# Optimization experiments

Measured on AMD Instinct MI355X. Metric: run time of the kernel, lower is better.

Reference implementation:

```python
import jax, jax.numpy as jnp
import numpy as np

N_HEADS = 16
D_EMBD = 1024
D_HEAD = D_EMBD // N_HEADS  # 64


def setup_inputs() -> dict:
    key = jax.random.key(0)
    k0, k1, k2, k3, k4 = jax.random.split(key, 5)
    s = 1.0 / np.sqrt(D_EMBD)
    return {
        "x": jax.random.normal(k0, (4, 2048, D_EMBD), dtype=jnp.float32),
        "w_in": jax.random.normal(k1, (D_EMBD, 3 * D_EMBD), dtype=jnp.float32) * s,
        "b_in": jax.random.normal(k2, (3 * D_EMBD,), dtype=jnp.float32) * 0.02,
        "w_out": jax.random.normal(k3, (D_EMBD, D_EMBD), dtype=jnp.float32) * s,
        "b_out": jax.random.normal(k4, (D_EMBD,), dtype=jnp.float32) * 0.02,
    }


def reference(x, w_in, b_in, w_out, b_out):
    B, S, D = x.shape
    # fused QKV projection; torch .chunk(3) order in source is k, q, v
    kqv = x @ w_in + b_in                      # [B, S, 3D]
    k, q, v = jnp.split(kqv, 3, axis=-1)
    # split heads: [B, S, D] -> [B, H, S, Dh]
    def heads(t):
        return t.reshape(B, S, N_HEADS, D_HEAD).transpose(0, 2, 1, 3)
    q, k, v = heads(q), heads(k), heads(v)
    # attention scores, explicit O(S^2) matrix (naive, unmasked path)
    scores = jnp.einsum("bhsd,bhtd->bhst", q, k) / jnp.sqrt(
        jnp.asarray(D_HEAD, dtype=x.dtype)
    )
    probs = jax.nn.softmax(scores, axis=-1)    # [B, H, S, S]
    out = jnp.einsum("bhst,bhtd->bhsd", probs, v)
    out = out.transpose(0, 2, 1, 3).reshape(B, S, D)
    return out @ w_out + b_out
```

## Files before the change

### kernel.cpp

```cpp
#include <hip/hip_runtime.h>

typedef unsigned short u16;
typedef __attribute__((ext_vector_type(8))) short bf16x8;
typedef __attribute__((ext_vector_type(4))) float f32x4;

#define MFMA(a, b, c) __builtin_amdgcn_mfma_f32_16x16x32_bf16(a, b, c, 0, 0, 0)

#if defined(__has_builtin)
#if __has_builtin(__builtin_amdgcn_exp2f)
#define EXP2(x) __builtin_amdgcn_exp2f(x)
#endif
#endif
#ifndef EXP2
#define EXP2(x) exp2f(x)
#endif

#define ASYNC16(g, l)                                                      \
  __builtin_amdgcn_global_load_lds(                                        \
      (const __attribute__((address_space(1))) void*)(g),                  \
      (__attribute__((address_space(3))) void*)(l), 16, 0, 0)

#define SEQ 2048
#define KQW 2048

__device__ __forceinline__ u16 f2bf(float x) {
  union { float f; unsigned u; } v; v.f = x;
  unsigned r = (v.u + 0x7fffu + ((v.u >> 16) & 1u)) >> 16;
  return (u16)r;
}

__device__ __forceinline__ unsigned pack_bf2(float a, float b) {
  unsigned ua = __float_as_uint(a) + 0x8000u;
  unsigned ub = __float_as_uint(b) + 0x8000u;
  return __builtin_amdgcn_perm(ub, ua, 0x07060302u);
}

__device__ __forceinline__ bf16x8 exp_pack8(const f32x4 a, const f32x4 b) {
  union { unsigned u[4]; bf16x8 v; } r;
  r.u[0] = pack_bf2(EXP2(a[0]), EXP2(a[1]));
  r.u[1] = pack_bf2(EXP2(a[2]), EXP2(a[3]));
  r.u[2] = pack_bf2(EXP2(b[0]), EXP2(b[1]));
  r.u[3] = pack_bf2(EXP2(b[2]), EXP2(b[3]));
  return r.v;
}

__global__ __launch_bounds__(256) void prep_fused(const float* __restrict__ w_in,
                                                  u16* __restrict__ wT_in,
                                                  const float* __restrict__ w_out,
                                                  u16* __restrict__ wT_out,
                                                  const float4* __restrict__ x,
                                                  uint2* __restrict__ xb) {
  int bid = blockIdx.x;
  int tid = threadIdx.x;
  if (bid >= 4096) {
    int idx = (bid - 4096) * 256 + tid;
    float4 v = x[idx];
    xb[idx] = make_uint2(pack_bf2(v.x, v.y), pack_bf2(v.z, v.w));
    return;
  }
  const float* in;
  u16* out;
  int R = 1024, C, bx, by;
  if (bid < 3072) {
    in = w_in; out = wT_in; C = 3072; bx = bid % 96; by = bid / 96;
  } else {
    int b2 = bid - 3072;
    in = w_out; out = wT_out; C = 1024; bx = b2 & 31; by = b2 >> 5;
  }
  __shared__ float tile[32][33];
  int tx = tid & 31, ty = tid >> 5;
  int c0 = bx * 32, r0 = by * 32;
#pragma unroll
  for (int i = 0; i < 32; i += 8)
    tile[ty + i][tx] = in[(size_t)(r0 + ty + i) * C + c0 + tx];
  __syncthreads();
#pragma unroll
  for (int i = 0; i < 32; i += 8)
    out[(size_t)(c0 + ty + i) * R + r0 + tx] = f2bf(tile[tx][ty + i]);
}

#define BM 128
#define BN 128
#define BK 64

template <int MODE, int NBX>
__global__ __launch_bounds__(256, 2) void gemm_bt(const u16* __restrict__ A,
                                                  const u16* __restrict__ Bt,
                                                  const float* __restrict__ bias,
                                                  void* __restrict__ Cout,
                                                  u16* __restrict__ vtout,
                                                  int M, int N, int K, int ldc,
                                                  int sc_lo, int sc_hi, float qs) {
  extern __shared__ __align__(16) u16 smem[];
  u16* As = smem;
  u16* Bs = smem + BM * BK;
  int id = blockIdx.x;
  int cpx = gridDim.x >> 3;
  int swz = (id & 7) * cpx + (id >> 3);
  int bn = (swz % NBX) * BN, bm = (swz / NBX) * BM;
  int tid = threadIdx.x;
  int wave = tid >> 6, lane = tid & 63;
  int quad = lane >> 4, l16 = lane & 15;
  int wm = (wave >> 1) * 64, wn = (wave & 1) * 64;

  f32x4 acc[4][4] = {};

  int lrow = lane >> 3, lcol = (lane & 7) * 8;
  const u16* gA = A + (size_t)(bm + wave * 8 + lrow) * K + lcol;
  const u16* gB = Bt + (size_t)(bn + wave * 8 + lrow) * K + lcol;
  u16* lA = &As[wave * 8 * BK];
  u16* lB = &Bs[wave * 8 * BK];

  for (int k0 = 0; k0 < K; k0 += BK) {
#pragma unroll
    for (int p = 0; p < 4; ++p) {
      ASYNC16(gA + (size_t)p * 32 * K, lA + p * 32 * BK);
      ASYNC16(gB + (size_t)p * 32 * K, lB + p * 32 * BK);
    }
    gA += BK;
    gB += BK;
    __syncthreads();
#pragma unroll
    for (int kk = 0; kk < BK; kk += 32) {
      bf16x8 af[4], bfr[4];
#pragma unroll
      for (int i = 0; i < 4; ++i)
        af[i] = *(const bf16x8*)&As[(wm + 16 * i + l16) * BK + kk + quad * 8];
#pragma unroll
      for (int j = 0; j < 4; ++j)
        bfr[j] = *(const bf16x8*)&Bs[(wn + 16 * j + l16) * BK + kk + quad * 8];
#pragma unroll
      for (int i = 0; i < 4; ++i)
#pragma unroll
        for (int j = 0; j < 4; ++j)
          acc[i][j] = MFMA(af[i], bfr[j], acc[i][j]);
    }
    __syncthreads();
  }

  if constexpr (MODE == 2) {
    if (bn >= 2048) {
      u16* vtile = smem;
#pragma unroll
      for (int j = 0; j < 4; ++j) {
        int vc = wn + 16 * j + l16;
        float bv = bias[bn + vc];
#pragma unroll
        for (int i = 0; i < 4; ++i) {
          u16 t4[4];
#pragma unroll
          for (int r = 0; r < 4; ++r) t4[r] = f2bf(acc[i][j][r] + bv);
          *(uint2*)&vtile[vc * 132 + wm + 16 * i + quad * 4] = *(uint2*)t4;
        }
      }
      __syncthreads();
      int b = bm >> 11, s0 = bm & 2047;
      int c = tid & 15, tt = c >> 3, c8 = c & 7;
      int B0 = 32 * (c8 >> 2) + 4 * (c8 & 3);
#pragma unroll
      for (int vgi = 0; vgi < 8; ++vgi) {
        int vc = vgi * 16 + (tid >> 4);
        int d = vc & 63;
        int bh = b * 16 + ((bn - 2048) >> 6) + (vc >> 6);
        const u16* src = &vtile[vc * 132 + tt * 64];
        u16 tmp[8];
        *(uint2*)&tmp[0] = *(const uint2*)&src[B0];
        *(uint2*)&tmp[4] = *(const uint2*)&src[B0 + 16];
        *(uint4*)&vtout[(size_t)bh * 64 * SEQ + (size_t)d * SEQ + s0 + c * 8] =
            *(uint4*)tmp;
      }
      return;
    }
  }

#pragma unroll
  for (int i = 0; i < 4; ++i) {
#pragma unroll
    for (int j = 0; j < 4; ++j) {
      int gn = bn + wn + 16 * j + l16;
      float bv = bias[gn];
      float sc = (gn >= sc_lo && gn < sc_hi) ? qs : 1.0f;
#pragma unroll
      for (int r = 0; r < 4; ++r) {
        int gm = bm + wm + 16 * i + quad * 4 + r;
        float v = (acc[i][j][r] + bv) * sc;
        if (MODE == 1)
          ((float*)Cout)[(size_t)gm * ldc + gn] = v;
        else
          ((u16*)Cout)[(size_t)gm * ldc + gn] = f2bf(v);
      }
    }
  }
}

__global__ __launch_bounds__(256, 4) void attn_kernel(const u16* __restrict__ kqv,
                                                      const u16* __restrict__ vt,
                                                      u16* __restrict__ out) {
  int g = blockIdx.x;
  int bh = g & 63, qtile = g >> 6;
  int b = bh >> 4, h = bh & 15;
  int tid = threadIdx.x, wave = tid >> 6, lane = tid & 63;
  int quad = lane >> 4, l16 = lane & 15;

  __shared__ __align__(16) u16 Ks[2][64 * 64];
  __shared__ __align__(16) u16 Vts[3][64 * 64];

  const u16* base = kqv + (size_t)b * SEQ * KQW;
  int hcol = h * 64;
  const u16* vbase = vt + (size_t)bh * 64 * SEQ;

  bf16x8 qf[2][2];
#pragma unroll
  for (int t = 0; t < 2; ++t) {
    int s = qtile * 128 + wave * 32 + t * 16 + l16;
    const u16* qrow = base + (size_t)s * KQW + 1024 + hcol;
    qf[t][0] = *(const bf16x8*)(qrow + quad * 8);
    qf[t][1] = *(const bf16x8*)(qrow + 32 + quad * 8);
  }

  bf16x8 ones;
#pragma unroll
  for (int i = 0; i < 8; ++i) ones[i] = (short)0x3F80;

  f32x4 o[2][4] = {};
  f32x4 ol[2] = {};
  const f32x4 zf = {};

  int prow = lane & 7;
  int pchk = (lane >> 3) * 8;

  int rb2 = (l16 >> 3) * 512;
  int r8 = (l16 & 7) * 8;

  const u16* kg = base + hcol + (size_t)(wave * 16 + prow) * KQW + pchk;
  const u16* vg = vbase + (size_t)(wave * 16 + prow) * SEQ + pchk;

#define STAGE_K(bi)                                      \
  do {                                                   \
    ASYNC16(kg, &Ks[bi][wave * 16 * 64]);                \
    ASYNC16(kg + (size_t)8 * KQW, &Ks[bi][(wave * 16 + 8) * 64]); \
    kg += (size_t)64 * KQW;                              \
  } while (0)
#define STAGE_V(bi)                                      \
  do {                                                   \
    ASYNC16(vg, &Vts[bi][wave * 16 * 64]);               \
    ASYNC16(vg + (size_t)8 * SEQ, &Vts[bi][(wave * 16 + 8) * 64]); \
    vg += 64;                                            \
  } while (0)

  const int NT = SEQ / 64;

  STAGE_K(0);
  STAGE_V(0);
  __syncthreads();
  STAGE_K(1);
  STAGE_V(1);

  bf16x8 pa00, pa01, pa10, pa11;
  {
    const u16* ks = &Ks[0][0];
    f32x4 s0[4], s1[4];
#pragma unroll
    for (int j = 0; j < 4; ++j) {
      bf16x8 k0 = *(const bf16x8*)&ks[j * 1024 + rb2 + quad * 64 + r8];
      bf16x8 k1 = *(const bf16x8*)&ks[j * 1024 + rb2 + 256 + quad * 64 + r8];
      s0[j] = MFMA(k0, qf[0][0], zf);
      s0[j] = MFMA(k1, qf[0][1], s0[j]);
      s1[j] = MFMA(k0, qf[1][0], zf);
      s1[j] = MFMA(k1, qf[1][1], s1[j]);
    }
    pa00 = exp_pack8(s0[0], s0[1]);
    pa01 = exp_pack8(s0[2], s0[3]);
    pa10 = exp_pack8(s1[0], s1[1]);
    pa11 = exp_pack8(s1[2], s1[3]);
  }

  int v_rd = 0;
  int v_st = 2;

  for (int t = 0; t < NT - 1; ++t) {
    __syncthreads();

    if (t + 2 < NT) {
      STAGE_K(t & 1);
      STAGE_V(v_st);
    }

    const u16* ks = &Ks[(t + 1) & 1][0];
    const u16* vs = &Vts[v_rd][0];

    __builtin_amdgcn_s_setprio(1);

    f32x4 s0[4], s1[4];
#pragma unroll
    for (int j = 0; j < 4; ++j) {
      bf16x8 k0 = *(const bf16x8*)&ks[j * 1024 + rb2 + quad * 64 + r8];
      bf16x8 k1 = *(const bf16x8*)&ks[j * 1024 + rb2 + 256 + quad * 64 + r8];
      s0[j] = MFMA(k0, qf[0][0], zf);
      s0[j] = MFMA(k1, qf[0][1], s0[j]);
      s1[j] = MFMA(k0, qf[1][0], zf);
      s1[j] = MFMA(k1, qf[1][1], s1[j]);
    }

    bf16x8 pn00 = exp_pack8(s0[0], s0[1]);
    bf16x8 pn01 = exp_pack8(s0[2], s0[3]);
    bf16x8 pn10 = exp_pack8(s1[0], s1[1]);
    bf16x8 pn11 = exp_pack8(s1[2], s1[3]);

#pragma unroll
    for (int d = 0; d < 4; ++d) {
      bf16x8 v0 = *(const bf16x8*)&vs[d * 1024 + rb2 + quad * 64 + r8];
      bf16x8 v1 = *(const bf16x8*)&vs[d * 1024 + rb2 + 256 + quad * 64 + r8];
      o[0][d] = MFMA(pa00, v0, o[0][d]);
      o[0][d] = MFMA(pa01, v1, o[0][d]);
      o[1][d] = MFMA(pa10, v0, o[1][d]);
      o[1][d] = MFMA(pa11, v1, o[1][d]);
    }
    ol[0] = MFMA(pa00, ones, ol[0]);
    ol[0] = MFMA(pa01, ones, ol[0]);
    ol[1] = MFMA(pa10, ones, ol[1]);
    ol[1] = MFMA(pa11, ones, ol[1]);

    __builtin_amdgcn_s_setprio(0);

    pa00 = pn00; pa01 = pn01; pa10 = pn10; pa11 = pn11;
    v_rd = (v_rd == 2) ? 0 : v_rd + 1;
    v_st = (v_st == 2) ? 0 : v_st + 1;
  }

  __syncthreads();
  {
    const u16* vs = &Vts[v_rd][0];
    __builtin_amdgcn_s_setprio(1);
#pragma unroll
    for (int d = 0; d < 4; ++d) {
      bf16x8 v0 = *(const bf16x8*)&vs[d * 1024 + rb2 + quad * 64 + r8];
      bf16x8 v1 = *(const bf16x8*)&vs[d * 1024 + rb2 + 256 + quad * 64 + r8];
      o[0][d] = MFMA(pa00, v0, o[0][d]);
      o[0][d] = MFMA(pa01, v1, o[0][d]);
      o[1][d] = MFMA(pa10, v0, o[1][d]);
      o[1][d] = MFMA(pa11, v1, o[1][d]);
    }
    ol[0] = MFMA(pa00, ones, ol[0]);
    ol[0] = MFMA(pa01, ones, ol[0]);
    ol[1] = MFMA(pa10, ones, ol[1]);
    ol[1] = MFMA(pa11, ones, ol[1]);
    __builtin_amdgcn_s_setprio(0);
  }

#pragma unroll
  for (int t = 0; t < 2; ++t)
#pragma unroll
    for (int r = 0; r < 4; ++r) {
      float inv = 1.0f / ol[t][r];
      int s = qtile * 128 + wave * 32 + t * 16 + quad * 4 + r;
      u16* orow = out + (size_t)(b * SEQ + s) * 1024 + hcol;
#pragma unroll
      for (int d = 0; d < 4; ++d) orow[16 * d + l16] = f2bf(o[t][d][r] * inv);
    }
#undef STAGE_K
#undef STAGE_V
}

extern "C" void kernel_launch(void* const* d_in, const int* in_sizes, int n_in,
                              void* d_out, int out_size, void* d_ws, size_t ws_size,
                              hipStream_t stream) {
  const float* x     = (const float*)d_in[0];
  const float* w_in  = (const float*)d_in[1];
  const float* b_in  = (const float*)d_in[2];
  const float* w_out = (const float*)d_in[3];
  const float* b_out = (const float*)d_in[4];
  float* outp = (float*)d_out;

  char* p = (char*)d_ws;
  u16* wT_in  = (u16*)p; p += (size_t)3072 * 1024 * 2;
  u16* wT_out = (u16*)p; p += (size_t)1024 * 1024 * 2;
  u16* xb     = (u16*)p; p += (size_t)8192 * 1024 * 2;
  u16* kqv    = (u16*)p; p += (size_t)8192 * 2048 * 2;
  u16* vtbuf  = (u16*)p; p += (size_t)64 * 64 * 2048 * 2;
  u16* attn   = (u16*)p;

  prep_fused<<<dim3(12288), dim3(256), 0, stream>>>(
      w_in, wT_in, w_out, wT_out, (const float4*)x, (uint2*)xb);

  const float QSCALE = 0.125f * 1.44269504088896f;
  gemm_bt<2, 3072 / BN><<<dim3((3072 / BN) * (8192 / BM)), 256, 33792, stream>>>(
      xb, wT_in, b_in, (void*)kqv, vtbuf, 8192, 3072, 1024, 2048, 1024, 2048, QSCALE);

  attn_kernel<<<dim3(1024), 256, 0, stream>>>(kqv, vtbuf, attn);

  gemm_bt<1, 1024 / BN><<<dim3((1024 / BN) * (8192 / BM)), 256, 32768, stream>>>(
      attn, wT_out, b_out, (void*)outp, nullptr, 8192, 1024, 1024, 1024, 0, 0, 1.0f);
}
```

Before: 263.0 us.

## Halve attention query tile, load V directly from global, drop software pipelining

The attention kernel now gives each wave 16 query rows instead of 32, so each block covers 64 rows and twice as many blocks are launched. The V^T tile is no longer staged through LDS; each lane reads its V fragments straight from global memory every iteration. The one-tile-ahead exp/MFMA software pipeline is removed, and launch bounds rise to 6 blocks per CU. The aim is more occupancy and less LDS and register pressure, at the cost of twice as many K/V reads per query and exposed global-load latency on V.

```diff
diff --git a/kernel.cpp b/kernel.cpp
--- a/kernel.cpp
+++ b/kernel.cpp
@@ -193,7 +193,7 @@
   }
 }
 
-__global__ __launch_bounds__(256, 4) void attn_kernel(const u16* __restrict__ kqv,
+__global__ __launch_bounds__(256, 6) void attn_kernel(const u16* __restrict__ kqv,
                                                       const u16* __restrict__ vt,
                                                       u16* __restrict__ out) {
   int g = blockIdx.x;
@@ -203,27 +203,25 @@
   int quad = lane >> 4, l16 = lane & 15;
 
   __shared__ __align__(16) u16 Ks[2][64 * 64];
-  __shared__ __align__(16) u16 Vts[3][64 * 64];
 
   const u16* base = kqv + (size_t)b * SEQ * KQW;
   int hcol = h * 64;
   const u16* vbase = vt + (size_t)bh * 64 * SEQ;
 
-  bf16x8 qf[2][2];
-#pragma unroll
-  for (int t = 0; t < 2; ++t) {
-    int s = qtile * 128 + wave * 32 + t * 16 + l16;
+  bf16x8 qf0, qf1;
+  {
+    int s = qtile * 64 + wave * 16 + l16;
     const u16* qrow = base + (size_t)s * KQW + 1024 + hcol;
-    qf[t][0] = *(const bf16x8*)(qrow + quad * 8);
-    qf[t][1] = *(const bf16x8*)(qrow + 32 + quad * 8);
+    qf0 = *(const bf16x8*)(qrow + quad * 8);
+    qf1 = *(const bf16x8*)(qrow + 32 + quad * 8);
   }
 
   bf16x8 ones;
 #pragma unroll
   for (int i = 0; i < 8; ++i) ones[i] = (short)0x3F80;
 
-  f32x4 o[2][4] = {};
-  f32x4 ol[2] = {};
+  f32x4 o[4] = {};
+  f32x4 ol = {};
   const f32x4 zf = {};
 
   int prow = lane & 7;
@@ -232,134 +230,69 @@
   int rb2 = (l16 >> 3) * 512;
   int r8 = (l16 & 7) * 8;
 
+  const u16* vlane = vbase + (size_t)(8 * (l16 >> 3) + (l16 & 7)) * SEQ + 8 * quad;
+
   const u16* kg = base + hcol + (size_t)(wave * 16 + prow) * KQW + pchk;
-  const u16* vg = vbase + (size_t)(wave * 16 + prow) * SEQ + pchk;
-
-#define STAGE_K(bi)                                      \
-  do {                                                   \
-    ASYNC16(kg, &Ks[bi][wave * 16 * 64]);                \
-    ASYNC16(kg + (size_t)8 * KQW, &Ks[bi][(wave * 16 + 8) * 64]); \
-    kg += (size_t)64 * KQW;                              \
-  } while (0)
-#define STAGE_V(bi)                                      \
-  do {                                                   \
-    ASYNC16(vg, &Vts[bi][wave * 16 * 64]);               \
-    ASYNC16(vg + (size_t)8 * SEQ, &Vts[bi][(wave * 16 + 8) * 64]); \
-    vg += 64;                                            \
-  } while (0)
-
-  const int NT = SEQ / 64;
-
-  STAGE_K(0);
-  STAGE_V(0);
-  __syncthreads();
-  STAGE_K(1);
-  STAGE_V(1);
-
-  bf16x8 pa00, pa01, pa10, pa11;
-  {
-    const u16* ks = &Ks[0][0];
-    f32x4 s0[4], s1[4];
+
+  ASYNC16(kg, &Ks[0][wave * 16 * 64]);
+  ASYNC16(kg + (size_t)8 * KQW, &Ks[0][(wave * 16 + 8) * 64]);
+
+  int cur = 0;
+
+  for (int t0 = 0; t0 < SEQ; t0 += 64) {
+    __syncthreads();
+
+    if (t0 + 64 < SEQ) {
+      kg += (size_t)64 * KQW;
+      ASYNC16(kg, &Ks[cur ^ 1][wave * 16 * 64]);
+      ASYNC16(kg + (size_t)8 * KQW, &Ks[cur ^ 1][(wave * 16 + 8) * 64]);
+    }
+
+    bf16x8 v0[4], v1[4];
+#pragma unroll
+    for (int d = 0; d < 4; ++d) {
+      const u16* vr = vlane + (size_t)(16 * d) * SEQ + t0;
+      v0[d] = *(const bf16x8*)(vr);
+      v1[d] = *(const bf16x8*)(vr + 32);
+    }
+
+    const u16* ks = &Ks[cur][0];
+
+    __builtin_amdgcn_s_setprio(1);
+
+    f32x4 s0[4];
 #pragma unroll
     for (int j = 0; j < 4; ++j) {
       bf16x8 k0 = *(const bf16x8*)&ks[j * 1024 + rb2 + quad * 64 + r8];
       bf16x8 k1 = *(const bf16x8*)&ks[j * 1024 + rb2 + 256 + quad * 64 + r8];
-      s0[j] = MFMA(k0, qf[0][0], zf);
-      s0[j] = MFMA(k1, qf[0][1], s0[j]);
-      s1[j] = MFMA(k0, qf[1][0], zf);
-      s1[j] = MFMA(k1, qf[1][1], s1[j]);
-    }
-    pa00 = exp_pack8(s0[0], s0[1]);
-    pa01 = exp_pack8(s0[2], s0[3]);
-    pa10 = exp_pack8(s1[0], s1[1]);
-    pa11 = exp_pack8(s1[2], s1[3]);
-  }
-
-  int v_rd = 0;
-  int v_st = 2;
-
-  for (int t = 0; t < NT - 1; ++t) {
-    __syncthreads();
-
-    if (t + 2 < NT) {
-      STAGE_K(t & 1);
-      STAGE_V(v_st);
-    }
-
-    const u16* ks = &Ks[(t + 1) & 1][0];
-    const u16* vs = &Vts[v_rd][0];
-
-    __builtin_amdgcn_s_setprio(1);
-
-    f32x4 s0[4], s1[4];
-#pragma unroll
-    for (int j = 0; j < 4; ++j) {
-      bf16x8 k0 = *(const bf16x8*)&ks[j * 1024 + rb2 + quad * 64 + r8];
-      bf16x8 k1 = *(const bf16x8*)&ks[j * 1024 + rb2 + 256 + quad * 64 + r8];
-      s0[j] = MFMA(k0, qf[0][0], zf);
-      s0[j] = MFMA(k1, qf[0][1], s0[j]);
-      s1[j] = MFMA(k0, qf[1][0], zf);
-      s1[j] = MFMA(k1, qf[1][1], s1[j]);
-    }
-
-    bf16x8 pn00 = exp_pack8(s0[0], s0[1]);
-    bf16x8 pn01 = exp_pack8(s0[2], s0[3]);
-    bf16x8 pn10 = exp_pack8(s1[0], s1[1]);
-    bf16x8 pn11 = exp_pack8(s1[2], s1[3]);
+      s0[j] = MFMA(k0, qf0, zf);
+      s0[j] = MFMA(k1, qf1, s0[j]);
+    }
+
+    bf16x8 pa0 = exp_pack8(s0[0], s0[1]);
+    bf16x8 pa1 = exp_pack8(s0[2], s0[3]);
 
 #pragma unroll
     for (int d = 0; d < 4; ++d) {
-      bf16x8 v0 = *(const bf16x8*)&vs[d * 1024 + rb2 + quad * 64 + r8];
-      bf16x8 v1 = *(const bf16x8*)&vs[d * 1024 + rb2 + 256 + quad * 64 + r8];
-      o[0][d] = MFMA(pa00, v0, o[0][d]);
-      o[0][d] = MFMA(pa01, v1, o[0][d]);
-      o[1][d] = MFMA(pa10, v0, o[1][d]);
-      o[1][d] = MFMA(pa11, v1, o[1][d]);
-    }
-    ol[0] = MFMA(pa00, ones, ol[0]);
-    ol[0] = MFMA(pa01, ones, ol[0]);
-    ol[1] = MFMA(pa10, ones, ol[1]);
-    ol[1] = MFMA(pa11, ones, ol[1]);
+      o[d] = MFMA(pa0, v0[d], o[d]);
+      o[d] = MFMA(pa1, v1[d], o[d]);
+    }
+    ol = MFMA(pa0, ones, ol);
+    ol = MFMA(pa1, ones, ol);
 
     __builtin_amdgcn_s_setprio(0);
 
-    pa00 = pn00; pa01 = pn01; pa10 = pn10; pa11 = pn11;
-    v_rd = (v_rd == 2) ? 0 : v_rd + 1;
-    v_st = (v_st == 2) ? 0 : v_st + 1;
-  }
-
-  __syncthreads();
-  {
-    const u16* vs = &Vts[v_rd][0];
-    __builtin_amdgcn_s_setprio(1);
-#pragma unroll
-    for (int d = 0; d < 4; ++d) {
-      bf16x8 v0 = *(const bf16x8*)&vs[d * 1024 + rb2 + quad * 64 + r8];
-      bf16x8 v1 = *(const bf16x8*)&vs[d * 1024 + rb2 + 256 + quad * 64 + r8];
-      o[0][d] = MFMA(pa00, v0, o[0][d]);
-      o[0][d] = MFMA(pa01, v1, o[0][d]);
-      o[1][d] = MFMA(pa10, v0, o[1][d]);
-      o[1][d] = MFMA(pa11, v1, o[1][d]);
-    }
-    ol[0] = MFMA(pa00, ones, ol[0]);
-    ol[0] = MFMA(pa01, ones, ol[0]);
-    ol[1] = MFMA(pa10, ones, ol[1]);
-    ol[1] = MFMA(pa11, ones, ol[1]);
-    __builtin_amdgcn_s_setprio(0);
-  }
-
-#pragma unroll
-  for (int t = 0; t < 2; ++t)
-#pragma unroll
-    for (int r = 0; r < 4; ++r) {
-      float inv = 1.0f / ol[t][r];
-      int s = qtile * 128 + wave * 32 + t * 16 + quad * 4 + r;
-      u16* orow = out + (size_t)(b * SEQ + s) * 1024 + hcol;
-#pragma unroll
-      for (int d = 0; d < 4; ++d) orow[16 * d + l16] = f2bf(o[t][d][r] * inv);
-    }
-#undef STAGE_K
-#undef STAGE_V
+    cur ^= 1;
+  }
+
+#pragma unroll
+  for (int r = 0; r < 4; ++r) {
+    float inv = 1.0f / ol[r];
+    int s = qtile * 64 + wave * 16 + quad * 4 + r;
+    u16* orow = out + (size_t)(b * SEQ + s) * 1024 + hcol;
+#pragma unroll
+    for (int d = 0; d < 4; ++d) orow[16 * d + l16] = f2bf(o[d][r] * inv);
+  }
 }
 
 extern "C" void kernel_launch(void* const* d_in, const int* in_sizes, int n_in,
@@ -387,7 +320,7 @@
   gemm_bt<2, 3072 / BN><<<dim3((3072 / BN) * (8192 / BM)), 256, 33792, stream>>>(
       xb, wT_in, b_in, (void*)kqv, vtbuf, 8192, 3072, 1024, 2048, 1024, 2048, QSCALE);
 
-  attn_kernel<<<dim3(1024), 256, 0, stream>>>(kqv, vtbuf, attn);
+  attn_kernel<<<dim3(2048), 256, 0, stream>>>(kqv, vtbuf, attn);
 
   gemm_bt<1, 1024 / BN><<<dim3((1024 / BN) * (8192 / BM)), 256, 32768, stream>>>(
       attn, wT_out, b_out, (void*)outp, nullptr, 8192, 1024, 1024, 1024, 0, 0, 1.0f);
```

New measurement: 544.3 us. 107% more time.
